# Performance work log

Measured on AMD Instinct MI355X. Metric: run time of the kernel, lower is better.

The kernel has to match this reference:

```python
import jax, jax.numpy as jnp
import numpy as np

B, S, DIM, HEADS = 4, 2048, 1024, 16
SCALE = float((DIM // HEADS) ** 0.5)  # sqrt(d_k) = 8.0
EPS = 1e-5


def _ln(h, g, b):
    m = jnp.mean(h, axis=-1, keepdims=True)
    v = jnp.mean((h - m) ** 2, axis=-1, keepdims=True)
    return (h - m) * jax.lax.rsqrt(v + EPS) * g + b


def setup_inputs() -> dict:
    key = jax.random.key(0)
    ks = jax.random.split(key, 16)
    w = lambda k: jax.random.normal(k, (DIM, DIM), jnp.float32) * 0.02
    vec = lambda k: jax.random.normal(k, (DIM,), jnp.float32) * 0.02
    return {
        "x": jax.random.normal(ks[0], (B, S, DIM), jnp.float32),
        "Wq": w(ks[1]), "bq": vec(ks[2]),
        "Wk": w(ks[3]), "bk": vec(ks[4]),
        "Wv": w(ks[5]), "bv": vec(ks[6]),
        "g_at": 1.0 + vec(ks[7]), "b_at": vec(ks[8]),
        "g_ln": 1.0 + vec(ks[9]), "b_ln": vec(ks[10]),
        "W1": w(ks[11]), "c1": vec(ks[12]),
        "W2": w(ks[13]), "c2": vec(ks[14]),
    }


def reference(x, Wq, bq, Wk, bk, Wv, bv, g_at, b_at, g_ln, b_ln, W1, c1, W2, c2):
    # --- MultiHeadAttention (single-head math: no head reshape in source) ---
    Q = x @ Wq + bq                                   # [B,S,D]
    K = x @ Wk + bk
    V = x @ Wv + bv
    scores = jax.nn.softmax(jnp.einsum('bqd,bkd->bqk', Q, K) / SCALE, axis=-1)
    at = _ln(jnp.einsum('bqk,bkd->bqd', scores, V) + x, g_at, b_at)
    # --- EncoderStack ---
    h = _ln(at + x, g_ln, b_ln)
    res = h
    # note: source's `if i != len(self.ffn)` is always True -> GELU on every layer
    h = jax.nn.gelu(h @ W1 + c1, approximate=False)
    h = jax.nn.gelu(h @ W2 + c2, approximate=False)
    return _ln(h + res, g_ln, b_ln)
```

## Files before the change

kernel.cpp:

```cpp
#include <hip/hip_runtime.h>
#include <cstdint>
#include <cstddef>

#define DIMN 1024
#define SEQ  2048
#define NBAT 4
#define TOKS (NBAT * SEQ)

typedef unsigned short u16;
typedef unsigned int   u32;

typedef __bf16 bf16x8 __attribute__((ext_vector_type(8)));
typedef float  f32x4  __attribute__((ext_vector_type(4)));

#define AS1 __attribute__((address_space(1)))
#define AS3 __attribute__((address_space(3)))


__device__ __forceinline__ u16 f2b(float f) {
  union { float f; u32 u; } v; v.f = f;
  u32 r = v.u + 0x7fffu + ((v.u >> 16) & 1u);
  return (u16)(r >> 16);
}

__device__ __forceinline__ float b2f(u16 b) {
  union { u32 u; float f; } v; v.u = ((u32)b) << 16;
  return v.f;
}

__device__ __forceinline__ float gelu_exact(float v) {
  return 0.5f * v * (1.0f + erff(v * 0.70710678118654752f));
}

__device__ __forceinline__ void blk_sum2(float& a, float& b, float* sm) {
  #pragma unroll
  for (int o = 32; o >= 1; o >>= 1) {
    a += __shfl_xor(a, o, 64);
    b += __shfl_xor(b, o, 64);
  }
  int w = threadIdx.x >> 6;
  if ((threadIdx.x & 63) == 0) { sm[w] = a; sm[4 + w] = b; }
  __syncthreads();
  a = sm[0] + sm[1] + sm[2] + sm[3];
  b = sm[4] + sm[5] + sm[6] + sm[7];
  __syncthreads();
}

__device__ __forceinline__ float blk_max(float a, float* sm) {
  #pragma unroll
  for (int o = 32; o >= 1; o >>= 1) a = fmaxf(a, __shfl_xor(a, o, 64));
  int w = threadIdx.x >> 6;
  if ((threadIdx.x & 63) == 0) sm[w] = a;
  __syncthreads();
  float r = fmaxf(fmaxf(sm[0], sm[1]), fmaxf(sm[2], sm[3]));
  __syncthreads();
  return r;
}

__device__ __forceinline__ float blk_sum1(float a, float* sm) {
  #pragma unroll
  for (int o = 32; o >= 1; o >>= 1) a += __shfl_xor(a, o, 64);
  int w = threadIdx.x >> 6;
  if ((threadIdx.x & 63) == 0) sm[w] = a;
  __syncthreads();
  float r = sm[0] + sm[1] + sm[2] + sm[3];
  __syncthreads();
  return r;
}


__global__ __launch_bounds__(256) void conv_x(const float* __restrict__ x,
                                              u16* __restrict__ xb) {
  size_t i = ((size_t)blockIdx.x * 256 + threadIdx.x) * 4;
  float4 v = *(const float4*)(x + i);
  uint2 o;
  o.x = (u32)f2b(v.x) | ((u32)f2b(v.y) << 16);
  o.y = (u32)f2b(v.z) | ((u32)f2b(v.w) << 16);
  *(uint2*)(xb + i) = o;
}

__global__ __launch_bounds__(256) void transpose_w5(
    const float* __restrict__ Wq, const float* __restrict__ Wk,
    const float* __restrict__ Wv, const float* __restrict__ W1,
    const float* __restrict__ W2,
    u16* __restrict__ Wqkv, u16* __restrict__ W1T, u16* __restrict__ W2T)
{
  const float* W; u16* T;
  switch (blockIdx.z) {
    case 0: W = Wq; T = Wqkv;                      break;
    case 1: W = Wk; T = Wqkv + 1 * DIMN * DIMN;    break;
    case 2: W = Wv; T = Wqkv + 2 * DIMN * DIMN;    break;
    case 3: W = W1; T = W1T;                       break;
    default: W = W2; T = W2T;                      break;
  }
  __shared__ float t[32][33];
  int tx = threadIdx.x, ty = threadIdx.y;
  int k0 = blockIdx.x * 32, n0 = blockIdx.y * 32;
  #pragma unroll
  for (int j = 0; j < 32; j += 8)
    t[ty + j][tx] = W[(size_t)(k0 + ty + j) * DIMN + n0 + tx];
  __syncthreads();
  #pragma unroll
  for (int j = 0; j < 32; j += 8)
    T[(size_t)(n0 + ty + j) * DIMN + k0 + tx] = f2b(t[tx][ty + j]);
}

__global__ __launch_bounds__(256) void transpose_v(const u16* __restrict__ Vb,
                                                   u16* __restrict__ VT) {
  __shared__ u16 t[32][33];
  int tx = threadIdx.x, ty = threadIdx.y;
  int d0 = blockIdx.x * 32, t0 = blockIdx.y * 32;
  const u16* src = Vb + (size_t)blockIdx.z * SEQ * DIMN;
  u16*       dst = VT + (size_t)blockIdx.z * DIMN * SEQ;
  #pragma unroll
  for (int j = 0; j < 32; j += 8)
    t[ty + j][tx] = src[(size_t)(t0 + ty + j) * DIMN + d0 + tx];
  __syncthreads();
  #pragma unroll
  for (int j = 0; j < 32; j += 8)
    dst[(size_t)(d0 + ty + j) * SEQ + t0 + tx] = t[tx][ty + j];
}

template <int EPI, int SWZ>
__global__ __launch_bounds__(256) void gemm_bt(
    const u16* __restrict__ A, const u16* __restrict__ Bm,
    u16* __restrict__ Cb, u16* __restrict__ Cb2, u16* __restrict__ Cb3,
    const float* __restrict__ bias, const float* __restrict__ bias2,
    const float* __restrict__ bias3,
    int M, int N, int K, int ldc,
    size_t sA, size_t sB, size_t sC)
{
  __shared__ u16 As[128 * 64];
  __shared__ u16 Bs[128 * 64];

  const int tid = threadIdx.x;

  int bm0, bn0;
  if (SWZ == 1) {
    const int id   = blockIdx.y * gridDim.x + blockIdx.x;
    const int xcd  = id & 7;
    const int idx  = id >> 3;
    const int band = gridDim.x >> 3;
    const int bm_l = idx % band;
    const int bn   = idx / band;
    bm0 = (xcd * band + bm_l) * 128;
    bn0 = bn * 128;
  } else {
    bm0 = blockIdx.x * 128;
    bn0 = blockIdx.y * 128;
  }

  A  += (size_t)blockIdx.z * sA;
  Bm += (size_t)blockIdx.z * sB;
  const int wave = tid >> 6, lane = tid & 63;
  const int wm   = (wave >> 1) * 64, wn = (wave & 1) * 64;
  const int l16  = lane & 15, quad = lane >> 4;

  f32x4 acc[4][4] = {};

  for (int k0 = 0; k0 < K; k0 += 64) {
    #pragma unroll
    for (int j = 0; j < 4; ++j) {
      const int c  = wave * 256 + j * 64 + lane;
      const int r  = c >> 3;
      const int cg = (c & 7) ^ (r & 7);
      const u16* gA = A  + (size_t)(bm0 + r) * K + k0 + cg * 8;
      const u16* gB = Bm + (size_t)(bn0 + r) * K + k0 + cg * 8;
      u16* lA = As + (wave * 4 + j) * 512;
      u16* lB = Bs + (wave * 4 + j) * 512;
      __builtin_amdgcn_global_load_lds((const AS1 void*)gA, (AS3 void*)lA, 16, 0, 0);
      __builtin_amdgcn_global_load_lds((const AS1 void*)gB, (AS3 void*)lB, 16, 0, 0);
    }
    __syncthreads();

    #pragma unroll
    for (int kk = 0; kk < 64; kk += 32) {
      const int kc = kk >> 3;
      const int sw = l16 & 7;
      bf16x8 af[4], bfr[4];
      #pragma unroll
      for (int t = 0; t < 4; ++t) {
        const int row = wm + t * 16 + l16;
        af[t] = *(const bf16x8*)(&As[row * 64 + (((kc + quad) ^ sw) << 3)]);
      }
      #pragma unroll
      for (int t = 0; t < 4; ++t) {
        const int row = wn + t * 16 + l16;
        bfr[t] = *(const bf16x8*)(&Bs[row * 64 + (((kc + quad) ^ sw) << 3)]);
      }
      #pragma unroll
      for (int mt = 0; mt < 4; ++mt)
        #pragma unroll
        for (int nt = 0; nt < 4; ++nt)
          acc[mt][nt] = __builtin_amdgcn_mfma_f32_16x16x32_bf16(
              af[mt], bfr[nt], acc[mt][nt], 0, 0, 0);
    }
    __syncthreads();
  }

  u16* Cbz = Cb + (size_t)blockIdx.z * sC;

  #pragma unroll
  for (int mt = 0; mt < 4; ++mt) {
    int grow0 = bm0 + wm + mt * 16 + quad * 4;
    #pragma unroll
    for (int nt = 0; nt < 4; ++nt) {
      int gcol = bn0 + wn + nt * 16 + l16;
      if (EPI == 3) {
        const int seg = gcol >> 10;
        const int col = gcol & 1023;
        const float* bp = (seg == 0) ? bias : (seg == 1) ? bias2 : bias3;
        u16*         cp = (seg == 0) ? Cb   : (seg == 1) ? Cb2   : Cb3;
        float bv = bp[col];
        #pragma unroll
        for (int r = 0; r < 4; ++r)
          cp[(size_t)(grow0 + r) * ldc + col] = f2b(acc[mt][nt][r] + bv);
      } else if (EPI == 4) {
        float bv = bias[gcol];
        #pragma unroll
        for (int r = 0; r < 4; ++r)
          Cbz[(size_t)(grow0 + r) * ldc + gcol] =
              f2b(gelu_exact(acc[mt][nt][r] + bv));
      } else {
        #pragma unroll
        for (int r = 0; r < 4; ++r)
          Cbz[(size_t)(grow0 + r) * ldc + gcol] = f2b(acc[mt][nt][r]);
      }
    }
  }
}

template <int EPI, int SWZ>
__global__ __launch_bounds__(512, 2) void gemm256(
    const u16* __restrict__ A, const u16* __restrict__ Bm,
    u16* __restrict__ Cb, u16* __restrict__ Cb2, u16* __restrict__ Cb3,
    const float* __restrict__ bias, const float* __restrict__ bias2,
    const float* __restrict__ bias3,
    int M, int N, int K, int ldc,
    size_t sA, size_t sB, size_t sC)
{
  __shared__ u16 AB[2][2][2][256 * 32];

  const int tid = threadIdx.x;

  int bm0, bn0;
  if (SWZ == 1) {
    const int id   = blockIdx.y * gridDim.x + blockIdx.x;
    const int xcd  = id & 7;
    const int idx  = id >> 3;
    const int band = gridDim.x >> 3;
    const int bm_l = idx % band;
    const int bn   = idx / band;
    bm0 = (xcd * band + bm_l) * 256;
    bn0 = bn * 256;
  } else {
    bm0 = blockIdx.x * 256;
    bn0 = blockIdx.y * 256;
  }

  A  += (size_t)blockIdx.z * sA;
  Bm += (size_t)blockIdx.z * sB;

  const int wave = tid >> 6, lane = tid & 63;
  const int wm   = (wave >> 2) * 128, wn = (wave & 3) * 64;
  const int l16  = lane & 15, quad = lane >> 4;
  const int rs8  = (quad ^ ((l16 >> 1) & 3)) << 3;
  const int cg8  = ((lane & 3) ^ ((lane >> 3) & 3)) << 3;
  const int srow = wave * 32 + (lane >> 2);

  f32x4 acc[8][4] = {};
  bf16x8 af[4], bf[4];

  const int nk  = K >> 6;
  const int nit = nk >> 1;

#define VM8() asm volatile("s_waitcnt vmcnt(8)" ::: "memory")
#define VM4() asm volatile("s_waitcnt vmcnt(4)" ::: "memory")
#define VM0() asm volatile("s_waitcnt vmcnt(0)" ::: "memory")
#define SBAR() __builtin_amdgcn_s_barrier()
#define SCHEDB() __builtin_amdgcn_sched_barrier(0)

#define STG(BUF, ABI, KH, KT) do {                                             \
    const u16* _P   = (ABI) ? Bm : A;                                          \
    const int _b0   = (ABI) ? bn0 : bm0;                                       \
    const int _kc   = (KT) * 64 + (KH) * 32;                                   \
    _Pragma("unroll")                                                          \
    for (int _j = 0; _j < 2; ++_j) {                                           \
      const u16* _g = _P + (size_t)(_b0 + srow + _j * 16) * K + _kc + cg8;     \
      u16* _l = &AB[BUF][ABI][KH][(wave * 128 + _j * 64) * 8];                 \
      __builtin_amdgcn_global_load_lds((const AS1 void*)_g, (AS3 void*)_l,     \
                                       16, 0, 0);                              \
    }                                                                          \
  } while (0)

#define LDA(BUF, KH, MH) do {                                                  \
    const u16* _u = &AB[BUF][0][KH][0];                                        \
    _Pragma("unroll")                                                          \
    for (int _i = 0; _i < 4; ++_i)                                             \
      af[_i] = *(const bf16x8*)(_u + (wm + (MH) * 64 + _i * 16 + l16) * 32     \
                                  + rs8);                                      \
  } while (0)

#define LDB(BUF, KH) do {                                                      \
    const u16* _u = &AB[BUF][1][KH][0];                                        \
    _Pragma("unroll")                                                          \
    for (int _i = 0; _i < 4; ++_i)                                             \
      bf[_i] = *(const bf16x8*)(_u + (wn + _i * 16 + l16) * 32 + rs8);         \
  } while (0)

#define MMCL(MH) do {                                                          \
    __builtin_amdgcn_s_setprio(1);                                             \
    _Pragma("unroll")                                                          \
    for (int _mt = 0; _mt < 4; ++_mt) {                                        \
      _Pragma("unroll")                                                        \
      for (int _nt = 0; _nt < 4; ++_nt)                                        \
        acc[(MH) * 4 + _mt][_nt] = __builtin_amdgcn_mfma_f32_16x16x32_bf16(    \
            af[_mt], bf[_nt], acc[(MH) * 4 + _mt][_nt], 0, 0, 0);              \
    }                                                                          \
    __builtin_amdgcn_s_setprio(0);                                             \
  } while (0)

  STG(0, 0, 0, 0); STG(0, 1, 0, 0);
  STG(0, 0, 1, 0); STG(0, 1, 1, 0);
  STG(1, 0, 0, 1); STG(1, 1, 0, 1);
  VM8(); SBAR(); SCHEDB();

  for (int i = 0; i < nit; ++i) {
    const int t1 = 2 * i + 1;
    const bool last = (i == nit - 1);

    LDA(0, 0, 0); LDB(0, 0);
    STG(1, 0, 1, t1);
    SBAR();
    MMCL(0);
    SBAR(); SCHEDB();

    LDA(0, 0, 1);
    STG(1, 1, 1, t1);
    SBAR();
    MMCL(1);
    VM8(); SBAR(); SCHEDB();

    LDA(0, 1, 0); LDB(0, 1);
    if (!last) STG(0, 0, 0, t1 + 1);
    SBAR();
    MMCL(0);
    SBAR(); SCHEDB();

    LDA(0, 1, 1);
    if (!last) STG(0, 1, 0, t1 + 1);
    SBAR();
    MMCL(1);
    if (last) VM4(); else VM8();
    SBAR(); SCHEDB();

    LDA(1, 0, 0); LDB(1, 0);
    if (!last) STG(0, 0, 1, t1 + 1);
    SBAR();
    MMCL(0);
    SBAR(); SCHEDB();

    LDA(1, 0, 1);
    if (!last) STG(0, 1, 1, t1 + 1);
    SBAR();
    MMCL(1);
    if (last) VM0(); else VM8();
    SBAR(); SCHEDB();

    LDA(1, 1, 0); LDB(1, 1);
    if (!last) STG(1, 0, 0, t1 + 2);
    SBAR();
    MMCL(0);
    SBAR(); SCHEDB();

    LDA(1, 1, 1);
    if (!last) STG(1, 1, 0, t1 + 2);
    SBAR();
    MMCL(1);
    if (!last) { VM8(); }
    SBAR(); SCHEDB();
  }

#undef VM8
#undef VM4
#undef VM0
#undef SBAR
#undef SCHEDB
#undef STG
#undef LDA
#undef LDB
#undef MMCL

  u16* Cbz = Cb + (size_t)blockIdx.z * sC;

  #pragma unroll
  for (int mt = 0; mt < 8; ++mt) {
    int grow0 = bm0 + wm + mt * 16 + quad * 4;
    #pragma unroll
    for (int nt = 0; nt < 4; ++nt) {
      int gcol = bn0 + wn + nt * 16 + l16;
      if (EPI == 3) {
        const int seg = gcol >> 10;
        const int col = gcol & 1023;
        const float* bp = (seg == 0) ? bias : (seg == 1) ? bias2 : bias3;
        u16*         cp = (seg == 0) ? Cb   : (seg == 1) ? Cb2   : Cb3;
        float bv = bp[col];
        #pragma unroll
        for (int r = 0; r < 4; ++r)
          cp[(size_t)(grow0 + r) * ldc + col] = f2b(acc[mt][nt][r] + bv);
      } else if (EPI == 4) {
        float bv = bias[gcol];
        #pragma unroll
        for (int r = 0; r < 4; ++r)
          Cbz[(size_t)(grow0 + r) * ldc + gcol] =
              f2b(gelu_exact(acc[mt][nt][r] + bv));
      } else {
        #pragma unroll
        for (int r = 0; r < 4; ++r)
          Cbz[(size_t)(grow0 + r) * ldc + gcol] = f2b(acc[mt][nt][r]);
      }
    }
  }
}

__global__ __launch_bounds__(256) void softmax_rows(const u16* __restrict__ Sc,
                                                    u16* __restrict__ P) {
  __shared__ float sm[8];
  int row = blockIdx.x, t = threadIdx.x;
  const u16* s = Sc + (size_t)row * SEQ;
  uint4 raw = *(const uint4*)(s + t * 8);
  float v[8];
  #pragma unroll
  for (int m = 0; m < 4; ++m) {
    u32 w = ((const u32*)&raw)[m];
    v[2 * m]     = b2f((u16)(w & 0xffff)) * 0.125f;
    v[2 * m + 1] = b2f((u16)(w >> 16)) * 0.125f;
  }
  float mx = -1e30f;
  #pragma unroll
  for (int i = 0; i < 8; ++i) mx = fmaxf(mx, v[i]);
  mx = blk_max(mx, sm);
  float sum = 0.0f;
  #pragma unroll
  for (int i = 0; i < 8; ++i) { v[i] = __expf(v[i] - mx); sum += v[i]; }
  sum = blk_sum1(sum, sm);
  float inv = 1.0f / sum;
  uint4 o;
  #pragma unroll
  for (int m = 0; m < 4; ++m)
    ((u32*)&o)[m] = (u32)f2b(v[2 * m] * inv) | ((u32)f2b(v[2 * m + 1] * inv) << 16);
  *(uint4*)(P + (size_t)row * SEQ + t * 8) = o;
}

__global__ __launch_bounds__(256) void ln1_fused(
    const u16* __restrict__ attn, const u16* __restrict__ xb,
    const float* __restrict__ g_at, const float* __restrict__ b_at,
    const float* __restrict__ g_ln, const float* __restrict__ b_ln,
    u16* __restrict__ hres)
{
  __shared__ float sm[8];
  int row = blockIdx.x, t = threadIdx.x;
  size_t base = (size_t)row * DIMN;
  uint2 ar = *(const uint2*)(attn + base + t * 4);
  uint2 xr4 = *(const uint2*)(xb + base + t * 4);
  float y[4], xr[4];
  float s = 0.0f, s2 = 0.0f;
  #pragma unroll
  for (int i = 0; i < 4; ++i) {
    u32 aw = ((const u32*)&ar)[i >> 1];
    u32 xw = ((const u32*)&xr4)[i >> 1];
    float av = b2f((u16)((i & 1) ? (aw >> 16) : (aw & 0xffff)));
    xr[i]    = b2f((u16)((i & 1) ? (xw >> 16) : (xw & 0xffff)));
    y[i] = av + xr[i];
    s += y[i]; s2 += y[i] * y[i];
  }
  blk_sum2(s, s2, sm);
  float m  = s * (1.0f / DIMN);
  float rs = rsqrtf(s2 * (1.0f / DIMN) - m * m + 1e-5f);
  float z[4];
  s = 0.0f; s2 = 0.0f;
  #pragma unroll
  for (int i = 0; i < 4; ++i) {
    int c = t * 4 + i;
    float at = (y[i] - m) * rs * g_at[c] + b_at[c];
    z[i] = at + xr[i];
    s += z[i]; s2 += z[i] * z[i];
  }
  blk_sum2(s, s2, sm);
  float m2  = s * (1.0f / DIMN);
  float rs2 = rsqrtf(s2 * (1.0f / DIMN) - m2 * m2 + 1e-5f);
  uint2 o;
  #pragma unroll
  for (int i = 0; i < 2; ++i) {
    int c = t * 4 + 2 * i;
    float h0 = (z[2 * i]     - m2) * rs2 * g_ln[c]     + b_ln[c];
    float h1 = (z[2 * i + 1] - m2) * rs2 * g_ln[c + 1] + b_ln[c + 1];
    ((u32*)&o)[i] = (u32)f2b(h0) | ((u32)f2b(h1) << 16);
  }
  *(uint2*)(hres + base + t * 4) = o;
}

__global__ __launch_bounds__(256) void ln2_final(
    const u16* __restrict__ u, const u16* __restrict__ hres,
    const float* __restrict__ g, const float* __restrict__ bb,
    float* __restrict__ out)
{
  __shared__ float sm[8];
  int row = blockIdx.x, t = threadIdx.x;
  size_t base = (size_t)row * DIMN;
  uint2 ur = *(const uint2*)(u + base + t * 4);
  uint2 hr = *(const uint2*)(hres + base + t * 4);
  float y[4];
  float s = 0.0f, s2 = 0.0f;
  #pragma unroll
  for (int i = 0; i < 4; ++i) {
    u32 uw = ((const u32*)&ur)[i >> 1];
    u32 hw = ((const u32*)&hr)[i >> 1];
    float uv = b2f((u16)((i & 1) ? (uw >> 16) : (uw & 0xffff)));
    float hv = b2f((u16)((i & 1) ? (hw >> 16) : (hw & 0xffff)));
    y[i] = uv + hv;
    s += y[i]; s2 += y[i] * y[i];
  }
  blk_sum2(s, s2, sm);
  float m  = s * (1.0f / DIMN);
  float rs = rsqrtf(s2 * (1.0f / DIMN) - m * m + 1e-5f);
  float4 o;
  o.x = (y[0] - m) * rs * g[t * 4 + 0] + bb[t * 4 + 0];
  o.y = (y[1] - m) * rs * g[t * 4 + 1] + bb[t * 4 + 1];
  o.z = (y[2] - m) * rs * g[t * 4 + 2] + bb[t * 4 + 2];
  o.w = (y[3] - m) * rs * g[t * 4 + 3] + bb[t * 4 + 3];
  *(float4*)(out + base + t * 4) = o;
}


extern "C" void kernel_launch(void* const* d_in, const int* in_sizes, int n_in,
                              void* d_out, int out_size, void* d_ws, size_t ws_size,
                              hipStream_t stream)
{
  const float* x    = (const float*)d_in[0];
  const float* Wq   = (const float*)d_in[1];
  const float* bq   = (const float*)d_in[2];
  const float* Wk   = (const float*)d_in[3];
  const float* bk   = (const float*)d_in[4];
  const float* Wv   = (const float*)d_in[5];
  const float* bv   = (const float*)d_in[6];
  const float* g_at = (const float*)d_in[7];
  const float* b_at = (const float*)d_in[8];
  const float* g_ln = (const float*)d_in[9];
  const float* b_ln = (const float*)d_in[10];
  const float* W1   = (const float*)d_in[11];
  const float* c1   = (const float*)d_in[12];
  const float* W2   = (const float*)d_in[13];
  const float* c2   = (const float*)d_in[14];
  float* out = (float*)d_out;

  char* ws = (char*)d_ws;
  const size_t MB = 1u << 20;
  u16* xb    = (u16*)(ws + 0 * MB);
  u16* W1T   = (u16*)(ws + 16 * MB);
  u16* W2T   = (u16*)(ws + 18 * MB);
  u16* WqkvT = (u16*)(ws + 20 * MB);
  u16* Qb    = (u16*)(ws + 26 * MB);
  u16* Kb    = (u16*)(ws + 42 * MB);
  u16* Vb    = (u16*)(ws + 58 * MB);
  u16* VT    = (u16*)(ws + 74 * MB);
  u16* Sc    = (u16*)(ws + 90 * MB);
  u16* attn  = (u16*)(ws + 90 * MB);
  u16* hres  = (u16*)(ws + 106 * MB);
  u16* Pb    = (u16*)(ws + 122 * MB);
  u16* tb    = Kb;
  u16* ub    = Vb;

  conv_x<<<(TOKS * DIMN) / 1024, 256, 0, stream>>>(x, xb);
  transpose_w5<<<dim3(32, 32, 5), dim3(32, 8), 0, stream>>>(
      Wq, Wk, Wv, W1, W2, WqkvT, W1T, W2T);

  gemm256<3, 1><<<dim3(32, 12), 512, 0, stream>>>(
      xb, WqkvT, Qb, Kb, Vb, bq, bk, bv,
      TOKS, 3 * DIMN, DIMN, DIMN, 0, 0, 0);

  transpose_v<<<dim3(32, 64, NBAT), dim3(32, 8), 0, stream>>>(Vb, VT);

  gemm256<6, 0><<<dim3(8, 8, NBAT), 512, 0, stream>>>(
      Qb, Kb, Sc, nullptr, nullptr, nullptr, nullptr, nullptr,
      SEQ, SEQ, DIMN, SEQ,
      (size_t)SEQ * DIMN, (size_t)SEQ * DIMN, (size_t)SEQ * SEQ);
  softmax_rows<<<TOKS, 256, 0, stream>>>(Sc, Pb);
  gemm_bt<6, 0><<<dim3(16, 8, NBAT), 256, 0, stream>>>(
      Pb, VT, attn, nullptr, nullptr, nullptr, nullptr, nullptr,
      SEQ, DIMN, SEQ, DIMN,
      (size_t)SEQ * SEQ, (size_t)DIMN * SEQ, (size_t)SEQ * DIMN);

  ln1_fused<<<TOKS, 256, 0, stream>>>(attn, xb, g_at, b_at, g_ln, b_ln, hres);

  gemm_bt<4, 1><<<dim3(64, 8), 256, 0, stream>>>(
      hres, W1T, tb, nullptr, nullptr, c1, nullptr, nullptr,
      TOKS, DIMN, DIMN, DIMN, 0, 0, 0);
  gemm_bt<4, 1><<<dim3(64, 8), 256, 0, stream>>>(
      tb, W2T, ub, nullptr, nullptr, c2, nullptr, nullptr,
      TOKS, DIMN, DIMN, DIMN, 0, 0, 0);

  ln2_final<<<TOKS, 256, 0, stream>>>(ub, hres, g_ln, b_ln, out);
}
```

Before: 379.7 us.

## Double-buffer the 128x128 GEMM with async LDS staging and prefetch

Rewrites the 128-tile GEMM used for P·V and both FFN projections. It now double-buffers LDS, split into two K-halves, so global-to-LDS loads for the next K tile are issued while MFMAs run on the current one. This replaces the old pattern of loading, doing a full barrier, then computing. It also adds launch_bounds(256,2) to target two blocks per CU. Separately, sched_barrier calls are removed from the 256-tile GEMM, which gives the compiler more freedom to schedule but could disturb the hand-ordered interleaving.

```diff
diff --git a/kernel.cpp b/kernel.cpp
--- a/kernel.cpp
+++ b/kernel.cpp
@@ -122,7 +122,7 @@
 }
 
 template <int EPI, int SWZ>
-__global__ __launch_bounds__(256) void gemm_bt(
+__global__ __launch_bounds__(256, 2) void gemm128p(
     const u16* __restrict__ A, const u16* __restrict__ Bm,
     u16* __restrict__ Cb, u16* __restrict__ Cb2, u16* __restrict__ Cb3,
     const float* __restrict__ bias, const float* __restrict__ bias2,
@@ -130,8 +130,7 @@
     int M, int N, int K, int ldc,
     size_t sA, size_t sB, size_t sC)
 {
-  __shared__ u16 As[128 * 64];
-  __shared__ u16 Bs[128 * 64];
+  __shared__ u16 AB[2][2][2][128 * 32];
 
   const int tid = threadIdx.x;
 
@@ -152,51 +151,92 @@
 
   A  += (size_t)blockIdx.z * sA;
   Bm += (size_t)blockIdx.z * sB;
+
   const int wave = tid >> 6, lane = tid & 63;
   const int wm   = (wave >> 1) * 64, wn = (wave & 1) * 64;
   const int l16  = lane & 15, quad = lane >> 4;
+  const int rs8  = (quad ^ ((l16 >> 1) & 3)) << 3;
+  const int cg8  = ((lane & 3) ^ ((lane >> 3) & 3)) << 3;
+  const int srow = wave * 32 + (lane >> 2);
 
   f32x4 acc[4][4] = {};
-
-  for (int k0 = 0; k0 < K; k0 += 64) {
-    #pragma unroll
-    for (int j = 0; j < 4; ++j) {
-      const int c  = wave * 256 + j * 64 + lane;
-      const int r  = c >> 3;
-      const int cg = (c & 7) ^ (r & 7);
-      const u16* gA = A  + (size_t)(bm0 + r) * K + k0 + cg * 8;
-      const u16* gB = Bm + (size_t)(bn0 + r) * K + k0 + cg * 8;
-      u16* lA = As + (wave * 4 + j) * 512;
-      u16* lB = Bs + (wave * 4 + j) * 512;
-      __builtin_amdgcn_global_load_lds((const AS1 void*)gA, (AS3 void*)lA, 16, 0, 0);
-      __builtin_amdgcn_global_load_lds((const AS1 void*)gB, (AS3 void*)lB, 16, 0, 0);
-    }
-    __syncthreads();
-
-    #pragma unroll
-    for (int kk = 0; kk < 64; kk += 32) {
-      const int kc = kk >> 3;
-      const int sw = l16 & 7;
-      bf16x8 af[4], bfr[4];
-      #pragma unroll
-      for (int t = 0; t < 4; ++t) {
-        const int row = wm + t * 16 + l16;
-        af[t] = *(const bf16x8*)(&As[row * 64 + (((kc + quad) ^ sw) << 3)]);
-      }
-      #pragma unroll
-      for (int t = 0; t < 4; ++t) {
-        const int row = wn + t * 16 + l16;
-        bfr[t] = *(const bf16x8*)(&Bs[row * 64 + (((kc + quad) ^ sw) << 3)]);
-      }
-      #pragma unroll
-      for (int mt = 0; mt < 4; ++mt)
-        #pragma unroll
-        for (int nt = 0; nt < 4; ++nt)
-          acc[mt][nt] = __builtin_amdgcn_mfma_f32_16x16x32_bf16(
-              af[mt], bfr[nt], acc[mt][nt], 0, 0, 0);
-    }
-    __syncthreads();
-  }
+  bf16x8 af[4], bf[4];
+
+  const int nk = K >> 6;
+
+#define VM4() asm volatile("s_waitcnt vmcnt(4)" ::: "memory")
+#define VM0() asm volatile("s_waitcnt vmcnt(0)" ::: "memory")
+#define SBAR() __builtin_amdgcn_s_barrier()
+
+#define STG(BUF, KH, KT) do {                                                  \
+    const int _kc = (KT) * 64 + (KH) * 32;                                     \
+    _Pragma("unroll")                                                          \
+    for (int _j = 0; _j < 2; ++_j) {                                           \
+      const u16* _gA = A  + (size_t)(bm0 + srow + _j * 16) * K + _kc + cg8;    \
+      const u16* _gB = Bm + (size_t)(bn0 + srow + _j * 16) * K + _kc + cg8;    \
+      u16* _lA = &AB[BUF][0][KH][(wave * 128 + _j * 64) * 8];                  \
+      u16* _lB = &AB[BUF][1][KH][(wave * 128 + _j * 64) * 8];                  \
+      __builtin_amdgcn_global_load_lds((const AS1 void*)_gA, (AS3 void*)_lA,   \
+                                       16, 0, 0);                              \
+      __builtin_amdgcn_global_load_lds((const AS1 void*)_gB, (AS3 void*)_lB,   \
+                                       16, 0, 0);                              \
+    }                                                                          \
+  } while (0)
+
+#define LDA(BUF, KH) do {                                                      \
+    const u16* _u = &AB[BUF][0][KH][0];                                        \
+    _Pragma("unroll")                                                          \
+    for (int _i = 0; _i < 4; ++_i)                                             \
+      af[_i] = *(const bf16x8*)(_u + (wm + _i * 16 + l16) * 32 + rs8);         \
+  } while (0)
+
+#define LDB(BUF, KH) do {                                                      \
+    const u16* _u = &AB[BUF][1][KH][0];                                        \
+    _Pragma("unroll")                                                          \
+    for (int _i = 0; _i < 4; ++_i)                                             \
+      bf[_i] = *(const bf16x8*)(_u + (wn + _i * 16 + l16) * 32 + rs8);         \
+  } while (0)
+
+#define MMCL() do {                                                            \
+    __builtin_amdgcn_s_setprio(1);                                             \
+    _Pragma("unroll")                                                          \
+    for (int _mt = 0; _mt < 4; ++_mt) {                                        \
+      _Pragma("unroll")                                                        \
+      for (int _nt = 0; _nt < 4; ++_nt)                                        \
+        acc[_mt][_nt] = __builtin_amdgcn_mfma_f32_16x16x32_bf16(               \
+            af[_mt], bf[_nt], acc[_mt][_nt], 0, 0, 0);                         \
+    }                                                                          \
+    __builtin_amdgcn_s_setprio(0);                                             \
+  } while (0)
+
+  STG(0, 0, 0);
+  STG(0, 1, 0);
+  VM4(); SBAR();
+
+  for (int t = 0; t < nk; ++t) {
+    const int buf = t & 1, nb = buf ^ 1;
+    const bool last = (t == nk - 1);
+
+    LDA(buf, 0); LDB(buf, 0);
+    if (!last) STG(nb, 0, t + 1);
+    MMCL();
+    if (last) VM0(); else VM4();
+    SBAR();
+
+    LDA(buf, 1); LDB(buf, 1);
+    if (!last) STG(nb, 1, t + 1);
+    MMCL();
+    if (!last) { VM4(); }
+    SBAR();
+  }
+
+#undef VM4
+#undef VM0
+#undef SBAR
+#undef STG
+#undef LDA
+#undef LDB
+#undef MMCL
 
   u16* Cbz = Cb + (size_t)blockIdx.z * sC;
 
@@ -278,7 +318,6 @@
 #define VM4() asm volatile("s_waitcnt vmcnt(4)" ::: "memory")
 #define VM0() asm volatile("s_waitcnt vmcnt(0)" ::: "memory")
 #define SBAR() __builtin_amdgcn_s_barrier()
-#define SCHEDB() __builtin_amdgcn_sched_barrier(0)
 
 #define STG(BUF, ABI, KH, KT) do {                                             \
     const u16* _P   = (ABI) ? Bm : A;                                          \
@@ -323,7 +362,7 @@
   STG(0, 0, 0, 0); STG(0, 1, 0, 0);
   STG(0, 0, 1, 0); STG(0, 1, 1, 0);
   STG(1, 0, 0, 1); STG(1, 1, 0, 1);
-  VM8(); SBAR(); SCHEDB();
+  VM8(); SBAR();
 
   for (int i = 0; i < nit; ++i) {
     const int t1 = 2 * i + 1;
@@ -333,59 +372,58 @@
     STG(1, 0, 1, t1);
     SBAR();
     MMCL(0);
-    SBAR(); SCHEDB();
+    SBAR();
 
     LDA(0, 0, 1);
     STG(1, 1, 1, t1);
     SBAR();
     MMCL(1);
-    VM8(); SBAR(); SCHEDB();
+    VM8(); SBAR();
 
     LDA(0, 1, 0); LDB(0, 1);
     if (!last) STG(0, 0, 0, t1 + 1);
     SBAR();
     MMCL(0);
-    SBAR(); SCHEDB();
+    SBAR();
 
     LDA(0, 1, 1);
     if (!last) STG(0, 1, 0, t1 + 1);
     SBAR();
     MMCL(1);
     if (last) VM4(); else VM8();
-    SBAR(); SCHEDB();
+    SBAR();
 
     LDA(1, 0, 0); LDB(1, 0);
     if (!last) STG(0, 0, 1, t1 + 1);
     SBAR();
     MMCL(0);
-    SBAR(); SCHEDB();
+    SBAR();
 
     LDA(1, 0, 1);
     if (!last) STG(0, 1, 1, t1 + 1);
     SBAR();
     MMCL(1);
     if (last) VM0(); else VM8();
-    SBAR(); SCHEDB();
+    SBAR();
 
     LDA(1, 1, 0); LDB(1, 1);
     if (!last) STG(1, 0, 0, t1 + 2);
     SBAR();
     MMCL(0);
-    SBAR(); SCHEDB();
+    SBAR();
 
     LDA(1, 1, 1);
     if (!last) STG(1, 1, 0, t1 + 2);
     SBAR();
     MMCL(1);
     if (!last) { VM8(); }
-    SBAR(); SCHEDB();
+    SBAR();
   }
 
 #undef VM8
 #undef VM4
 #undef VM0
 #undef SBAR
-#undef SCHEDB
 #undef STG
 #undef LDA
 #undef LDB
@@ -586,17 +624,18 @@
       SEQ, SEQ, DIMN, SEQ,
       (size_t)SEQ * DIMN, (size_t)SEQ * DIMN, (size_t)SEQ * SEQ);
   softmax_rows<<<TOKS, 256, 0, stream>>>(Sc, Pb);
-  gemm_bt<6, 0><<<dim3(16, 8, NBAT), 256, 0, stream>>>(
+
+  gemm128p<6, 0><<<dim3(16, 8, NBAT), 256, 0, stream>>>(
       Pb, VT, attn, nullptr, nullptr, nullptr, nullptr, nullptr,
       SEQ, DIMN, SEQ, DIMN,
       (size_t)SEQ * SEQ, (size_t)DIMN * SEQ, (size_t)SEQ * DIMN);
 
   ln1_fused<<<TOKS, 256, 0, stream>>>(attn, xb, g_at, b_at, g_ln, b_ln, hres);
 
-  gemm_bt<4, 1><<<dim3(64, 8), 256, 0, stream>>>(
+  gemm128p<4, 1><<<dim3(64, 8), 256, 0, stream>>>(
       hres, W1T, tb, nullptr, nullptr, c1, nullptr, nullptr,
       TOKS, DIMN, DIMN, DIMN, 0, 0, 0);
-  gemm_bt<4, 1><<<dim3(64, 8), 256, 0, stream>>>(
+  gemm128p<4, 1><<<dim3(64, 8), 256, 0, stream>>>(
       tb, W2T, ub, nullptr, nullptr, c2, nullptr, nullptr,
       TOKS, DIMN, DIMN, DIMN, 0, 0, 0);
 
```

Result: faster. 362.6 us (-4.5%).
